# Optimization experiments

Hardware: AMD Instinct MI355X
Metric: run time of the kernel (lower is better)

## Reference

```python
import jax, jax.numpy as jnp
import numpy as np

NEG_SLOPE = 0.2
EPS = 1e-08


def conv3d_same(x, w, b):
    # x: [b,c,d,h,w], w: [o,c,kd,kh,kw], stride 1, pad SAME (==pad 1 for k=3)
    y = jax.lax.conv_general_dilated(x, w, (1, 1, 1), 'SAME',
                                     dimension_numbers=('NCDHW', 'OIDHW', 'NCDHW'))
    return y + b[None, :, None, None, None]


def get_bl(frame):
    # frame: [b,3,h,w]; replicates numpy median/mean/std stats from get_BL
    x = jnp.clip(frame, 0.0, 1.0) * 255.0
    bsz = x.shape[0]
    r_med = jnp.median(x[:, 0].reshape(bsz, -1), axis=1)          # [b]
    g_mean = jnp.mean(x[:, 1], axis=(1, 2))
    g_std = jnp.std(x[:, 1], axis=(1, 2))                          # ddof=0, like np.std
    b_mean = jnp.mean(x[:, 2], axis=(1, 2))
    b_std = jnp.std(x[:, 2], axis=(1, 2))
    bl_r = 140.0 / (1.0 + 14.4 * jnp.exp(-0.034 * r_med))
    bl_g = 1.13 * g_mean + 1.11 * g_std - 25.6
    bl_b = 1.13 * b_mean + 1.11 * b_std - 25.6
    bl = jnp.stack([bl_r, bl_g, bl_b], axis=1)                     # [b,3]
    bl = jnp.clip(bl, 5.0, 250.0) / 255.0
    h, w = frame.shape[2], frame.shape[3]
    return jnp.broadcast_to(bl[:, :, None, None], (bsz, 3, h, w))


def leaky(x):
    return jnp.where(x >= 0, x, NEG_SLOPE * x)


def reference(i, j, w_bl1, b_bl1, w_bl2, b_bl2, w_t1, b_t1, w_t2, b_t2, w1, w2, t_bias):
    T = i.shape[2]
    # background light from the center frame (detached in the original)
    bl2d = jax.lax.stop_gradient(get_bl(i[:, :, T // 2]))          # [b,3,h,w]
    bl = jnp.broadcast_to(bl2d[:, :, None], i.shape)               # [b,3,T,h,w]
    j5 = jnp.broadcast_to(j[:, :, None], i.shape)                  # [b,3,T,h,w]
    # AdaptiveAvgPool3d((T,1,1)) == mean over h,w keeping frames
    diff = jnp.mean(i - j5, axis=(3, 4), keepdims=True)            # [b,3,T,1,1]
    # bl_ca: two 1x1x1 convs == channel-mixing matmuls
    h1 = leaky(jnp.einsum('bcdhw,oc->bodhw', diff, w_bl1[:, :, 0, 0, 0])
               + b_bl1[None, :, None, None, None])
    bl_diff = jax.nn.sigmoid(jnp.einsum('bcdhw,oc->bodhw', h1, w_bl2[:, :, 0, 0, 0])
                             + b_bl2[None, :, None, None, None])   # [b,3,T,1,1]
    bl = bl + w1 * bl_diff                                         # broadcast over h,w
    t3 = (i - bl) / (j5 - bl + EPS)
    x = i + w2 * t3
    h2 = leaky(conv3d_same(x, w_t1, b_t1))                         # [b,16,T,h,w]
    t = jax.nn.sigmoid(conv3d_same(h2, w_t2, b_t2)) + t_bias       # [b,1,T,h,w]
    return bl, t


def setup_inputs() -> dict:
    key = jax.random.key(0)
    ks = jax.random.split(key, 12)
    b, c, T, h, w = 4, 3, 5, 512, 512
    nf = 16
    inp = {
        'i': jax.random.uniform(ks[0], (b, c, T, h, w), dtype=jnp.float32),
        'j': jax.random.uniform(ks[1], (b, c, h, w), dtype=jnp.float32),
        'w_bl1': jax.random.normal(ks[2], (nf, 3, 1, 1, 1), dtype=jnp.float32) * 0.1,
        'b_bl1': jnp.zeros((nf,), jnp.float32),
        'w_bl2': jax.random.normal(ks[3], (3, nf, 1, 1, 1), dtype=jnp.float32) * 0.1,
        'b_bl2': jnp.zeros((3,), jnp.float32),
        'w_t1': jax.random.normal(ks[4], (nf, 3, 3, 3, 3), dtype=jnp.float32) * 0.1,
        'b_t1': jnp.zeros((nf,), jnp.float32),
        'w_t2': jax.random.normal(ks[5], (1, nf, 3, 3, 3), dtype=jnp.float32) * 0.1,
        'b_t2': jnp.zeros((1,), jnp.float32),
        'w1': jnp.zeros((1,), jnp.float32),
        'w2': jnp.zeros((1,), jnp.float32),
        't_bias': jnp.zeros((1, 1, T, 1, 1), jnp.float32),
    }
    return inp
```

## Files before the change

### kernel.cpp

```cpp
#include <hip/hip_runtime.h>

typedef unsigned int uint;
typedef unsigned short ushort;
typedef short bf16x8 __attribute__((ext_vector_type(8)));
typedef _Float16 f16x8 __attribute__((ext_vector_type(8)));
typedef float f32x4 __attribute__((ext_vector_type(4)));

#define NEG_SLOPE 0.2f

#define WS_HIST 0
#define WS_DBL  65536
#define WS_BLV  (WS_DBL + 704)
#define WS_WA   (WS_BLV + 256)
#define WS_W2A  (WS_WA + 4096)
#define WS_ZERO_BYTES (WS_DBL + 704)

#define HCH 24
#define HROW 432
#define HBUF 7776

__device__ __forceinline__ float leakyf(float x) { return fmaxf(x, NEG_SLOPE * x); }

__device__ __forceinline__ ushort f2bf(float f) {
  uint u = __float_as_uint(f);
  uint r = u + 0x7FFFu + ((u >> 16) & 1u);
  return (ushort)(r >> 16);
}
__device__ __forceinline__ uint cvt_pk_u32(float a, float b) {
  union { __fp16 __attribute__((ext_vector_type(2))) h; uint u; } c;
  c.h = __builtin_amdgcn_cvt_pkrtz(a, b);
  return c.u;
}
__device__ __forceinline__ uint cvt_pk_bf16(float a, float b) {
  uint r;
  asm("v_cvt_pk_bf16_f32 %0, %1, %2" : "=v"(r) : "v"(a), "v"(b));
  return r;
}

__global__ __launch_bounds__(256) void stats_kernel(const float* __restrict__ gi,
                                                    const float* __restrict__ gj,
                                                    double* __restrict__ sums,
                                                    uint* __restrict__ hist) {
  __shared__ double red[256];
  __shared__ uint lh[4096];
  const int plane = blockIdx.y;
  const int chunk = blockIdx.x;
  const int tid = threadIdx.x;

  if (plane >= 60) {
    const int jp = plane - 60;
    const float4* base = (const float4*)(gj + (size_t)jp * 262144);
    double dsum = 0.0;
    for (int k = 0; k < 8; ++k) {
      float4 v = base[chunk * 2048 + k * 256 + tid];
      dsum += (double)v.x + (double)v.y + (double)v.z + (double)v.w;
    }
    red[tid] = dsum; __syncthreads();
    for (int off = 128; off > 0; off >>= 1) { if (tid < off) red[tid] += red[tid + off]; __syncthreads(); }
    if (tid == 0) atomicAdd(&sums[60 + jp], red[0]);
    return;
  }

  const int b = plane / 15;
  const int rem = plane % 15;
  const int c = rem / 5;
  const int t = rem % 5;
  const float4* base = (const float4*)(gi + (size_t)plane * 262144);
  const bool dostat = (c >= 1 && t == 2);
  const bool domed = (c == 0 && t == 2);
  if (domed) {
    for (int i = tid; i < 4096; i += 256) lh[i] = 0;
    __syncthreads();
  }
  double dsum = 0.0, dsx = 0.0, dsx2 = 0.0;
  for (int k = 0; k < 8; ++k) {
    float4 v = base[chunk * 2048 + k * 256 + tid];
    dsum += (double)v.x + (double)v.y + (double)v.z + (double)v.w;
    if (dostat || domed) {
      float arr[4] = {v.x, v.y, v.z, v.w};
#pragma unroll
      for (int q = 0; q < 4; ++q) {
        float x = fminf(fmaxf(arr[q], 0.f), 1.f) * 255.f;
        if (domed) {
          int bin = (int)(x * (4096.0f / 255.0f));
          if (bin > 4095) bin = 4095;
          atomicAdd(&lh[bin], 1u);
        } else {
          dsx += (double)x;
          dsx2 += (double)x * (double)x;
        }
      }
    }
  }
  red[tid] = dsum; __syncthreads();
  for (int off = 128; off > 0; off >>= 1) { if (tid < off) red[tid] += red[tid + off]; __syncthreads(); }
  if (tid == 0) atomicAdd(&sums[plane], red[0]);
  __syncthreads();
  if (dostat) {
    red[tid] = dsx; __syncthreads();
    for (int off = 128; off > 0; off >>= 1) { if (tid < off) red[tid] += red[tid + off]; __syncthreads(); }
    if (tid == 0) atomicAdd(&sums[72 + b * 2 + (c - 1)], red[0]);
    __syncthreads();
    red[tid] = dsx2; __syncthreads();
    for (int off = 128; off > 0; off >>= 1) { if (tid < off) red[tid] += red[tid + off]; __syncthreads(); }
    if (tid == 0) atomicAdd(&sums[80 + b * 2 + (c - 1)], red[0]);
  }
  if (domed) {
    for (int i = tid; i < 4096; i += 256) { uint v = lh[i]; if (v) atomicAdd(&hist[b * 4096 + i], v); }
  }
}

__global__ void setup_kernel(const float* __restrict__ w_t1, const float* __restrict__ w_t2,
                             ushort* __restrict__ wA, ushort* __restrict__ w2A) {
  const int tid = threadIdx.x;
  for (int idx = tid; idx < 2048; idx += 256) {
    int o = idx >> 7, k = idx & 127, g = k >> 2, kw = k & 3;
    float v = 0.f;
    if (g < 27 && kw < 3) {
      int ci = g / 9, kd = (g % 9) / 3, kh = g % 3;
      v = w_t1[o * 81 + ci * 27 + kd * 9 + kh * 3 + kw];
    }
    wA[idx] = f2bf(v);
  }
  for (int idx = tid; idx < 12800; idx += 256) {
    int j = idx & 7;
    int lane = (idx >> 3) & 63;
    int rest = idx >> 9;
    int step = rest % 5;
    int tf = rest / 5;
    int ln = lane & 15, kb = lane >> 4;
    int k = kb * 8 + j;
    int tap = step * 2 + (k >> 4);
    int ch = k & 15;
    float v = 0.f;
    if (ln < 5 && tap < 9) {
      int kd = tf + 1 - ln;
      if (kd >= 0 && kd <= 2) v = w_t2[ch * 27 + kd * 9 + tap];
    }
    union { ushort s; _Float16 h; } cv; cv.h = (_Float16)v;
    w2A[idx] = cv.s;
  }
}

__global__ __launch_bounds__(256) void finalize_kernel(const uint* __restrict__ hist,
                                const double* __restrict__ sums,
                                const float* __restrict__ w_bl1, const float* __restrict__ b_bl1,
                                const float* __restrict__ w_bl2, const float* __restrict__ b_bl2,
                                const float* __restrict__ w1, float* __restrict__ blv) {
  __shared__ uint s[256];
  __shared__ float fv[2];
  __shared__ float rmed_s[4];
  const int tid = threadIdx.x;
  for (int b = 0; b < 4; ++b) {
    const uint* h = hist + b * 4096;
    uint loc[16]; uint part = 0;
#pragma unroll
    for (int q = 0; q < 16; ++q) { loc[q] = h[tid * 16 + q]; part += loc[q]; }
    s[tid] = part; __syncthreads();
    for (int off = 1; off < 256; off <<= 1) {
      uint v = (tid >= off) ? s[tid - off] : 0u;
      __syncthreads(); s[tid] += v; __syncthreads();
    }
    uint pref = s[tid] - part;
#pragma unroll
    for (int m = 0; m < 2; ++m) {
      uint k = 131071u + (uint)m;
      if (k >= pref && k < pref + part) {
        uint cum = pref;
        for (int q = 0; q < 16; ++q) {
          if (k < cum + loc[q]) { fv[m] = ((float)(tid * 16 + q) + 0.5f) * (255.f / 4096.f); break; }
          cum += loc[q];
        }
      }
    }
    __syncthreads();
    if (tid == 0) rmed_s[b] = 0.5f * (fv[0] + fv[1]);
    __syncthreads();
  }
  if (tid < 20) {
    const int b = tid / 5, t = tid % 5;
    const double inv = 1.0 / 262144.0;
    float bl2[3];
    bl2[0] = 140.f / (1.f + 14.4f * expf(-0.034f * rmed_s[b]));
    for (int c = 1; c < 3; ++c) {
      double m = sums[72 + b * 2 + (c - 1)] * inv;
      double ex2 = sums[80 + b * 2 + (c - 1)] * inv;
      double var = ex2 - m * m;
      if (var < 0.0) var = 0.0;
      bl2[c] = (float)(1.13 * m + 1.11 * sqrt(var) - 25.6);
    }
#pragma unroll
    for (int c = 0; c < 3; ++c)
      bl2[c] = fminf(fmaxf(bl2[c], 5.f), 250.f) * (1.f / 255.f);
    float diff[3];
    for (int c = 0; c < 3; ++c)
      diff[c] = (float)((sums[(b * 3 + c) * 5 + t] - sums[60 + b * 3 + c]) * inv);
    float h1[16];
    for (int o = 0; o < 16; ++o) {
      float sv = b_bl1[o];
      for (int c = 0; c < 3; ++c) sv += w_bl1[o * 3 + c] * diff[c];
      h1[o] = leakyf(sv);
    }
    const float w1v = w1[0];
    for (int c = 0; c < 3; ++c) {
      float sv = b_bl2[c];
      for (int o = 0; o < 16; ++o) sv += w_bl2[c * 16 + o] * h1[o];
      float sg = 1.f / (1.f + expf(-sv));
      blv[(b * 3 + c) * 5 + t] = bl2[c] + w1v * sg;
    }
  }
}

__global__ __launch_bounds__(256, 4) void fused_kernel(
    const float* __restrict__ gi, const float* __restrict__ gj,
    const ushort* __restrict__ wAg, const float* __restrict__ b_t1,
    const ushort* __restrict__ w2Ag, const float* __restrict__ b_t2,
    const float* __restrict__ w2p, const float* __restrict__ t_bias,
    const float* __restrict__ blv, float* __restrict__ out) {
  __shared__ __align__(16) ushort xsh[10560];
  __shared__ __align__(16) ushort h2sh[2 * HBUF];
  __shared__ __align__(16) int baseTab[160];
  __shared__ float blv_s[15];

  const int b = blockIdx.z;
  const int lin = blockIdx.y * 32 + blockIdx.x;
  const int swz = (lin & 7) * 128 + (lin >> 3);
  const int tY = swz >> 5, tX = swz & 31;
  const int tid = threadIdx.x;
  const int wv = tid >> 6;
  const int lane = tid & 63;
  const int ln = lane & 15;
  const int kb = lane >> 4;
  const int ty = tid >> 4, tx = tid & 15;
  const int gy = tY * 16 + ty, gx = tX * 16 + tx;
  const int ybase = tY * 16 - 2, xbase = tX * 16 - 2;

  if (tid < 15) blv_s[tid] = blv[b * 15 + tid];
  for (int i = tid; i < 5280; i += 256) ((uint*)xsh)[i] = 0u;
  if (tid < 160) {
    int tf_ = tid >> 5, kb_ = (tid >> 3) & 3, e = tid & 7;
    int g = (e >> 1) * 8 + kb_ * 2 + (e & 1);
    int sl = 3, sb = 0;
    if (g < 27) {
      int ci = g / 9, r9 = g % 9, kd = r9 / 3, kh = r9 % 3;
      sb = ci * 440 + kh * 22;
      int f = tf_ + kd - 1;
      sl = (f < 0) ? 3 : (f > 4) ? 1 : (f & 3);
    }
    baseTab[tid] = sb + sl * 1320;
  }

  union { uint4 u; bf16x8 v; } a4[4];
#pragma unroll
  for (int m = 0; m < 4; ++m)
    a4[m].u = *(const uint4*)(wAg + ln * 128 + m * 32 + kb * 8);
  f32x4 bias4;
#pragma unroll
  for (int r = 0; r < 4; ++r) bias4[r] = b_t1[kb * 4 + r];

  int pT[6];
  uint tmask = 0;
#pragma unroll
  for (int i = 0; i < 6; ++i) {
    int tile = wv + i * 4;
    int pos = tile * 16 + ln;
    int pe = pos < 324 ? pos : 323;
    int y0 = pe / 18, x0 = pe - y0 * 18;
    int p = x0 & 1;
    pT[i] = (y0 * 22 + x0 - p + p * 5280) | (pe << 13);
    int gyh = tY * 16 - 1 + y0, gxh = tX * 16 - 1 + x0;
    if (pos < 324) tmask |= 1u << i;
    if (gyh >= 0 && gyh < 512 && gxh >= 0 && gxh < 512) tmask |= 1u << (i + 8);
  }

  int bOff[5];
#pragma unroll
  for (int s = 0; s < 5; ++s) {
    int tap = s * 2 + (kb >> 1); if (tap > 8) tap = 8;
    int kh = tap / 3, kw = tap - kh * 3;
    bOff[s] = kh * HROW + kw * HCH + (kb & 1) * 8 + ln * HCH;
  }

  int qi3[3], eb3[3];
  uint civ3 = 0;
  float jv3[6];
  uint vmask = 0;
#pragma unroll
  for (int k = 0; k < 3; ++k) {
    int p = tid + k * 256;
    int pc = p < 600 ? p : 0;
    int ci = pc / 200, rem = pc - ci * 200;
    int ys = rem / 10, xp = rem - ys * 10;
    int gyy = ybase + ys, gxx = xbase + 2 * xp;
    bool inrow = (p < 600) && gyy >= 0 && gyy < 512;
    bool v0 = inrow && gxx >= 0 && gxx < 512;
    bool v1 = inrow && (gxx + 1) >= 0 && (gxx + 1) < 512;
    int cy = gyy < 0 ? 0 : (gyy > 511 ? 511 : gyy);
    int cx = gxx < 0 ? 0 : (gxx > 510 ? 510 : gxx);
    int spc = cy * 512 + cx;
    qi3[k] = (b * 3 + ci) * 1310720 + spc;
    float2 jp = *(const float2*)(gj + (b * 3 + ci) * 262144 + spc);
    jv3[k * 2] = jp.x; jv3[k * 2 + 1] = jp.y;
    eb3[k] = ci * 440 + ys * 22 + 2 * xp;
    civ3 |= (uint)(ci * 5) << (k * 4);
    if (v0) vmask |= 1u << (2 * k);
    if (v1) vmask |= 1u << (2 * k + 1);
    if (xp > 0) vmask |= 1u << (8 + k);
  }

  const float w2v = w2p[0];

  auto issue_loads = [&](int f, float2* ivr) {
    const int fo = f * 262144;
    ivr[0] = *(const float2*)(gi + qi3[0] + fo);
    ivr[1] = *(const float2*)(gi + qi3[1] + fo);
    ivr[2] = (tid < 88) ? *(const float2*)(gi + qi3[2] + fo) : make_float2(0.f, 0.f);
  };
  auto stage_frame = [&](int f, const float2* ivr) {
    const int sb2 = (f & 3) * 1320;
#pragma unroll
    for (int k = 0; k < 3; ++k) {
      if (k == 2 && tid >= 88) break;
      float bv = blv_s[((civ3 >> (k * 4)) & 15u) + f];
      float iv0 = ivr[k].x, iv1 = ivr[k].y;
      float x0 = ((vmask >> (2 * k)) & 1u)
                   ? fmaf(w2v, (iv0 - bv) * __builtin_amdgcn_rcpf(jv3[k * 2] - bv + 1e-8f), iv0) : 0.f;
      float x1 = ((vmask >> (2 * k + 1)) & 1u)
                   ? fmaf(w2v, (iv1 - bv) * __builtin_amdgcn_rcpf(jv3[k * 2 + 1] - bv + 1e-8f), iv1) : 0.f;
      uint pk = cvt_pk_bf16(x0, x1);
      int ebb = sb2 + eb3[k];
      *(uint*)(xsh + ebb) = pk;
      if ((vmask >> (8 + k)) & 1u) xsh[ebb + 5279] = (ushort)pk;
      xsh[ebb + 5280] = (ushort)(pk >> 16);
    }
  };
  auto stage_zero = [&](int slot) {
    const int sb2 = slot * 1320;
#pragma unroll
    for (int k = 0; k < 3; ++k) {
      if (k == 2 && tid >= 88) break;
      int ebb = sb2 + eb3[k];
      *(uint*)(xsh + ebb) = 0u;
      if ((vmask >> (8 + k)) & 1u) xsh[ebb + 5279] = 0;
      xsh[ebb + 5280] = 0;
    }
  };

  float2 ivr0[3], ivr1[3];
  issue_loads(0, ivr0);
  issue_loads(1, ivr1);

  __syncthreads();

#pragma unroll
  for (int c = 0; c < 3; ++c)
#pragma unroll
    for (int t = 0; t < 5; ++t)
      out[(((b * 3 + c) * 5 + t) * 512 + gy) * 512 + gx] = blv_s[c * 5 + t];

  stage_frame(0, ivr0);
  stage_frame(1, ivr1);
  __syncthreads();

  f32x4 acc2[4];
#pragma unroll
  for (int u = 0; u < 4; ++u) acc2[u] = (f32x4){0.f, 0.f, 0.f, 0.f};

#pragma unroll
  for (int tf = 0; tf < 5; ++tf) {
    float2 ivr[3];
    if (tf < 3) issue_loads(tf + 2, ivr);

    int4 bE0 = *(const int4*)&baseTab[tf * 32 + kb * 8];
    int4 bE1 = *(const int4*)&baseTab[tf * 32 + kb * 8 + 4];

    ushort* h2w = h2sh + (tf & 1) * HBUF;
    __builtin_amdgcn_s_setprio(1);
#pragma unroll
    for (int i = 0; i < 6; ++i) {
      if (i == 5 && wv != 0) continue;
      const int pT_ = pT[i];
      const int q = pT_ & 8191;
      f32x4 acc = bias4;
#pragma unroll
      for (int m = 0; m < 4; ++m) {
        int be0 = (m == 0) ? bE0.x : (m == 1) ? bE0.z : (m == 2) ? bE1.x : bE1.z;
        int be1 = (m == 0) ? bE0.y : (m == 1) ? bE0.w : (m == 2) ? bE1.y : bE1.w;
        const uint* p0 = (const uint*)(xsh + (be0 + q));
        const uint* p1 = (const uint*)(xsh + (be1 + q));
        union { uint4 u; bf16x8 v; } bfr;
        bfr.u = make_uint4(p0[0], p0[1], p1[0], p1[1]);
        acc = __builtin_amdgcn_mfma_f32_16x16x32_bf16(a4[m].v, bfr.v, acc, 0, 0, 0);
      }
      const bool inimg = (tmask >> (i + 8)) & 1u;
      float r0 = inimg ? leakyf(acc[0]) : 0.f;
      float r1 = inimg ? leakyf(acc[1]) : 0.f;
      float r2 = inimg ? leakyf(acc[2]) : 0.f;
      float r3 = inimg ? leakyf(acc[3]) : 0.f;
      uint p0 = cvt_pk_u32(r0, r1);
      uint p1 = cvt_pk_u32(r2, r3);
      if ((tmask >> i) & 1u)
        *(uint2*)(h2w + ((pT_ >> 13) * HCH + kb * 4)) = make_uint2(p0, p1);
    }
    __builtin_amdgcn_s_setprio(0);

    if (tf > 0) {
      const ushort* h2r = h2sh + ((tf - 1) & 1) * HBUF;
      const ushort* wbase = w2Ag + (tf - 1) * 5 * 64 * 8;
      __builtin_amdgcn_s_setprio(1);
#pragma unroll
      for (int s = 0; s < 5; ++s) {
        union { uint4 u; f16x8 v; } aw;
        aw.u = *(const uint4*)(wbase + (s * 64 + lane) * 8);
#pragma unroll
        for (int u = 0; u < 4; ++u) {
          const ushort* hb = h2r + (wv + u * 4) * HROW;
          union { uint4 u4; f16x8 v; } bfr;
          bfr.u4 = *(const uint4*)(hb + bOff[s]);
          acc2[u] = __builtin_amdgcn_mfma_f32_16x16x32_f16(aw.v, bfr.v, acc2[u], 0, 0, 0);
        }
      }
      __builtin_amdgcn_s_setprio(0);
    }

    if (tf < 3) stage_frame(tf + 2, ivr);
    else if (tf == 3) stage_zero(1);
    __syncthreads();
  }

  {
    const ushort* h2r = h2sh + 0 * HBUF;
    const ushort* wbase = w2Ag + 4 * 5 * 64 * 8;
#pragma unroll
    for (int s = 0; s < 5; ++s) {
      union { uint4 u; f16x8 v; } aw;
      aw.u = *(const uint4*)(wbase + (s * 64 + lane) * 8);
#pragma unroll
      for (int u = 0; u < 4; ++u) {
        const ushort* hb = h2r + (wv + u * 4) * HROW;
        union { uint4 u4; f16x8 v; } bfr;
        bfr.u4 = *(const uint4*)(hb + bOff[s]);
        acc2[u] = __builtin_amdgcn_mfma_f32_16x16x32_f16(aw.v, bfr.v, acc2[u], 0, 0, 0);
      }
    }
  }

  float* sredf = (float*)xsh;
#pragma unroll
  for (int u = 0; u < 4; ++u) {
    const int tt = wv + u * 4;
    if (kb == 0) {
#pragma unroll
      for (int r = 0; r < 4; ++r)
        sredf[r * 256 + tt * 16 + ln] = acc2[u][r];
    } else if (kb == 1) {
      sredf[4 * 256 + tt * 16 + ln] = acc2[u][0];
    }
  }
  __syncthreads();

  const float bt2 = b_t2[0];
#pragma unroll
  for (int t = 0; t < 5; ++t) {
    float tv = 1.f / (1.f + __expf(-(sredf[t * 256 + tid] + bt2))) + t_bias[t];
    out[15728640 + ((b * 5 + t) * 512 + gy) * 512 + gx] = tv;
  }
}

extern "C" void kernel_launch(void* const* d_in, const int* in_sizes, int n_in,
                              void* d_out, int out_size, void* d_ws, size_t ws_size,
                              hipStream_t stream) {
  const float* gi = (const float*)d_in[0];
  const float* gj = (const float*)d_in[1];
  const float* w_bl1 = (const float*)d_in[2];
  const float* b_bl1 = (const float*)d_in[3];
  const float* w_bl2 = (const float*)d_in[4];
  const float* b_bl2 = (const float*)d_in[5];
  const float* w_t1 = (const float*)d_in[6];
  const float* b_t1 = (const float*)d_in[7];
  const float* w_t2 = (const float*)d_in[8];
  const float* b_t2 = (const float*)d_in[9];
  const float* w1 = (const float*)d_in[10];
  const float* w2 = (const float*)d_in[11];
  const float* t_bias = (const float*)d_in[12];
  float* out = (float*)d_out;
  char* ws = (char*)d_ws;

  uint* hist = (uint*)(ws + WS_HIST);
  double* sums = (double*)(ws + WS_DBL);
  float* blv = (float*)(ws + WS_BLV);
  ushort* wA = (ushort*)(ws + WS_WA);
  ushort* w2A = (ushort*)(ws + WS_W2A);

  hipMemsetAsync(ws, 0, WS_ZERO_BYTES, stream);

  setup_kernel<<<1, 256, 0, stream>>>(w_t1, w_t2, wA, w2A);
  stats_kernel<<<dim3(32, 72), 256, 0, stream>>>(gi, gj, sums, hist);
  finalize_kernel<<<1, 256, 0, stream>>>(hist, sums, w_bl1, b_bl1, w_bl2, b_bl2, w1, blv);
  fused_kernel<<<dim3(32, 32, 4), 256, 0, stream>>>(gi, gj, wA, b_t1, w2A, b_t2, w2, t_bias, blv, out);
}
```

Baseline: 154.0 us.

## Single-buffer h2 in LDS and use 3-slot frame ring to cut shared memory

```diff
diff --git a/kernel.cpp b/kernel.cpp
--- a/kernel.cpp
+++ b/kernel.cpp
@@ -17,7 +17,6 @@
 
 #define HCH 24
 #define HROW 432
-#define HBUF 7776
 
 __device__ __forceinline__ float leakyf(float x) { return fmaxf(x, NEG_SLOPE * x); }
 
@@ -218,7 +217,7 @@
     const float* __restrict__ w2p, const float* __restrict__ t_bias,
     const float* __restrict__ blv, float* __restrict__ out) {
   __shared__ __align__(16) ushort xsh[10560];
-  __shared__ __align__(16) ushort h2sh[2 * HBUF];
+  __shared__ __align__(16) ushort h2sh[324 * HCH];
   __shared__ __align__(16) int baseTab[160];
   __shared__ float blv_s[15];
 
@@ -245,7 +244,7 @@
       int ci = g / 9, r9 = g % 9, kd = r9 / 3, kh = r9 % 3;
       sb = ci * 440 + kh * 22;
       int f = tf_ + kd - 1;
-      sl = (f < 0) ? 3 : (f > 4) ? 1 : (f & 3);
+      if (f >= 0 && f <= 4) sl = f % 3;
     }
     baseTab[tid] = sb + sl * 1320;
   }
@@ -317,7 +316,8 @@
     ivr[2] = (tid < 88) ? *(const float2*)(gi + qi3[2] + fo) : make_float2(0.f, 0.f);
   };
   auto stage_frame = [&](int f, const float2* ivr) {
-    const int sb2 = (f & 3) * 1320;
+    const int slot = (f >= 3) ? f - 3 : f;
+    const int sb2 = slot * 1320;
 #pragma unroll
     for (int k = 0; k < 3; ++k) {
       if (k == 2 && tid >= 88) break;
@@ -334,17 +334,6 @@
       xsh[ebb + 5280] = (ushort)(pk >> 16);
     }
   };
-  auto stage_zero = [&](int slot) {
-    const int sb2 = slot * 1320;
-#pragma unroll
-    for (int k = 0; k < 3; ++k) {
-      if (k == 2 && tid >= 88) break;
-      int ebb = sb2 + eb3[k];
-      *(uint*)(xsh + ebb) = 0u;
-      if ((vmask >> (8 + k)) & 1u) xsh[ebb + 5279] = 0;
-      xsh[ebb + 5280] = 0;
-    }
-  };
 
   float2 ivr0[3], ivr1[3];
   issue_loads(0, ivr0);
@@ -374,7 +363,6 @@
     int4 bE0 = *(const int4*)&baseTab[tf * 32 + kb * 8];
     int4 bE1 = *(const int4*)&baseTab[tf * 32 + kb * 8 + 4];
 
-    ushort* h2w = h2sh + (tf & 1) * HBUF;
     __builtin_amdgcn_s_setprio(1);
 #pragma unroll
     for (int i = 0; i < 6; ++i) {
@@ -400,13 +388,13 @@
       uint p0 = cvt_pk_u32(r0, r1);
       uint p1 = cvt_pk_u32(r2, r3);
       if ((tmask >> i) & 1u)
-        *(uint2*)(h2w + ((pT_ >> 13) * HCH + kb * 4)) = make_uint2(p0, p1);
+        *(uint2*)(h2sh + ((pT_ >> 13) * HCH + kb * 4)) = make_uint2(p0, p1);
     }
     __builtin_amdgcn_s_setprio(0);
-
-    if (tf > 0) {
-      const ushort* h2r = h2sh + ((tf - 1) & 1) * HBUF;
-      const ushort* wbase = w2Ag + (tf - 1) * 5 * 64 * 8;
+    __syncthreads();
+
+    {
+      const ushort* wbase = w2Ag + tf * 5 * 64 * 8;
       __builtin_amdgcn_s_setprio(1);
 #pragma unroll
       for (int s = 0; s < 5; ++s) {
@@ -414,7 +402,7 @@
         aw.u = *(const uint4*)(wbase + (s * 64 + lane) * 8);
 #pragma unroll
         for (int u = 0; u < 4; ++u) {
-          const ushort* hb = h2r + (wv + u * 4) * HROW;
+          const ushort* hb = h2sh + (wv + u * 4) * HROW;
           union { uint4 u4; f16x8 v; } bfr;
           bfr.u4 = *(const uint4*)(hb + bOff[s]);
           acc2[u] = __builtin_amdgcn_mfma_f32_16x16x32_f16(aw.v, bfr.v, acc2[u], 0, 0, 0);
@@ -424,25 +412,7 @@
     }
 
     if (tf < 3) stage_frame(tf + 2, ivr);
-    else if (tf == 3) stage_zero(1);
-    __syncthreads();
-  }
-
-  {
-    const ushort* h2r = h2sh + 0 * HBUF;
-    const ushort* wbase = w2Ag + 4 * 5 * 64 * 8;
-#pragma unroll
-    for (int s = 0; s < 5; ++s) {
-      union { uint4 u; f16x8 v; } aw;
-      aw.u = *(const uint4*)(wbase + (s * 64 + lane) * 8);
-#pragma unroll
-      for (int u = 0; u < 4; ++u) {
-        const ushort* hb = h2r + (wv + u * 4) * HROW;
-        union { uint4 u4; f16x8 v; } bfr;
-        bfr.u4 = *(const uint4*)(hb + bOff[s]);
-        acc2[u] = __builtin_amdgcn_mfma_f32_16x16x32_f16(aw.v, bfr.v, acc2[u], 0, 0, 0);
-      }
-    }
+    __syncthreads();
   }
 
   float* sredf = (float*)xsh;
```

Result: faster. 146.1 us (median of 2 runs) (-5.2%).
